# Performance work log

Measured on AMD Instinct MI355X. Metric: run time of the kernel, lower is better.

The kernel has to match this reference:

```python
import jax, jax.numpy as jnp
import numpy as np

N = 100000
E = 1600000
IN_DIM, HID_DIM, LAT_DIM = 256, 128, 64


def glorot(key, shape):
    lim = float(np.sqrt(6.0 / (shape[0] + shape[1])))
    return jax.random.uniform(key, shape, jnp.float32, -lim, lim)


def setup_inputs() -> dict:
    key = jax.random.key(0)
    ks = jax.random.split(key, 8)
    x = jax.random.normal(ks[0], (N, IN_DIM), jnp.float32)
    edge_index = jax.random.randint(ks[1], (2, E), 0, N, jnp.int64)
    return {
        "x": x,
        "edge_index": edge_index,
        "W1": glorot(ks[2], (IN_DIM, HID_DIM)),
        "b1": jnp.zeros((HID_DIM,), jnp.float32),
        "Wmu": glorot(ks[3], (HID_DIM, LAT_DIM)),
        "bmu": jnp.zeros((LAT_DIM,), jnp.float32),
        "Wls": glorot(ks[4], (HID_DIM, LAT_DIM)),
        "bls": jnp.zeros((LAT_DIM,), jnp.float32),
    }


def gcn_conv(x, src, dst, norm, W, b, n_nodes):
    # PyG GCNConv: linear transform, then symmetric-normalized scatter-add
    h = x @ W                                   # [N, out]
    msg = h[src] * norm[:, None]                # [E+N, out] gathered messages
    out = jax.ops.segment_sum(msg, dst, num_segments=n_nodes)
    return out + b


def reference(x, edge_index, W1, b1, Wmu, bmu, Wls, bls):
    # add self-loops (GCNConv default)
    loop = jnp.arange(N, dtype=edge_index.dtype)
    src = jnp.concatenate([edge_index[0], loop])
    dst = jnp.concatenate([edge_index[1], loop])
    # symmetric degree normalization: deg computed on target nodes
    deg = jax.ops.segment_sum(jnp.ones_like(dst, jnp.float32), dst, num_segments=N)
    dinv = jnp.where(deg > 0, jax.lax.rsqrt(jnp.maximum(deg, 1.0)), 0.0)
    norm = dinv[src] * dinv[dst]                # [E+N]

    h = jax.nn.relu(gcn_conv(x, src, dst, norm, W1, b1, N))
    mu = gcn_conv(h, src, dst, norm, Wmu, bmu, N)
    logstd = gcn_conv(h, src, dst, norm, Wls, bls, N)
    return (mu, logstd)
```

## Files before the change

### kernel.cpp

```cpp
#include <hip/hip_runtime.h>

#define IN_DIM 256
#define HID    128
#define LAT    64
#define SLOTS  64
#define RANGE  200
#define MAXBKT 512

typedef __attribute__((ext_vector_type(8))) short short8;
typedef __attribute__((ext_vector_type(4))) float floatx4;
typedef __attribute__((ext_vector_type(4))) int  intx4;
typedef __attribute__((ext_vector_type(2))) int  intx2;

static __device__ __forceinline__ ushort f2bf(float f) {
    union { float f; uint u; } v; v.f = f;
    uint u = v.u;
    uint r = (u + 0x7fffu + ((u >> 16) & 1u)) >> 16;
    return (ushort)r;
}
static __device__ __forceinline__ float bf_lo(uint v) { return __uint_as_float(v << 16); }
static __device__ __forceinline__ float bf_hi(uint v) { return __uint_as_float(v & 0xffff0000u); }

__global__ __launch_bounds__(256) void scatter_gemm1_kernel(
        const int* __restrict__ src, const int* __restrict__ dst,
        int* __restrict__ bkt, int* __restrict__ bkt_cnt,
        int cap, int nbkt, int E, int sblocks,
        const float* __restrict__ X, const ushort* __restrict__ W1T,
        ushort* __restrict__ O, int N) {
    __shared__ __align__(16) char smem[28 * 1024];

    if ((int)blockIdx.x < sblocks) {
        int* cntL  = (int*)smem;
        int* baseL = cntL + MAXBKT;
        int* posL  = baseL + MAXBKT;
        const int t = threadIdx.x;
        for (int b = t; b < nbkt; b += 256) { cntL[b] = 0; posL[b] = 0; }
        __syncthreads();
        const int e0 = blockIdx.x * 2048 + t * 8;
        int s[8], d[8];
        if (e0 + 7 < E) {
            *(int4*)(s)     = *(const int4*)(src + e0);
            *(int4*)(s + 4) = *(const int4*)(src + e0 + 4);
            *(int4*)(d)     = *(const int4*)(dst + e0);
            *(int4*)(d + 4) = *(const int4*)(dst + e0 + 4);
        } else {
            #pragma unroll
            for (int k = 0; k < 8; ++k) {
                int e = e0 + k;
                s[k] = (e < E) ? src[e] : 0;
                d[k] = (e < E) ? dst[e] : -1;
            }
        }
        int r[8];
        #pragma unroll
        for (int k = 0; k < 8; ++k) {
            r[k] = (d[k] >= 0) ? (d[k] / RANGE) : -1;
            if (r[k] >= 0) atomicAdd(&cntL[r[k]], 1);
        }
        __syncthreads();
        for (int b = t; b < nbkt; b += 256) {
            int c = cntL[b];
            baseL[b] = c ? atomicAdd(&bkt_cnt[b], c) : 0;
        }
        __syncthreads();
        #pragma unroll
        for (int k = 0; k < 8; ++k) {
            if (r[k] >= 0) {
                int off = atomicAdd(&posL[r[k]], 1);
                int p = baseL[r[k]] + off;
                if (p < cap) {
                    *(intx2*)(bkt + ((size_t)r[k] * cap + p) * 2) =
                        (intx2){s[k], d[k]};
                }
            }
        }
        return;
    }

    ushort* As = (ushort*)smem;
    ushort* Bs = As + 64 * 32;
    ushort* Cs = Bs + 128 * 32;
    const int bid  = blockIdx.x - sblocks;
    const int tid  = threadIdx.x;
    const int wave = tid >> 6, lane = tid & 63;
    const int q = lane >> 4, ln = lane & 15;
    const int row0 = bid * 64;
    floatx4 acc[8] = {};

    for (int k0 = 0; k0 < IN_DIM; k0 += 32) {
        #pragma unroll
        for (int t = 0; t < 2; ++t) {
            int j = t * 256 + tid;
            int r = j >> 3, kc = (j & 7) * 4;
            float4 v = make_float4(0.f, 0.f, 0.f, 0.f);
            if (row0 + r < N)
                v = *(const float4*)(X + (size_t)(row0 + r) * IN_DIM + k0 + kc);
            *(ushort4*)(As + r * 32 + kc) =
                make_ushort4(f2bf(v.x), f2bf(v.y), f2bf(v.z), f2bf(v.w));
        }
        #pragma unroll
        for (int t = 0; t < 2; ++t) {
            int c = t * 256 + tid;
            int n = c >> 2, kc = (c & 3) * 8;
            *(int4*)(Bs + n * 32 + kc) = *(const int4*)(W1T + (size_t)n * IN_DIM + k0 + kc);
        }
        __syncthreads();
        short8 a = *(const short8*)(As + (wave * 16 + ln) * 32 + q * 8);
        #pragma unroll
        for (int t = 0; t < 8; ++t) {
            short8 b = *(const short8*)(Bs + (t * 16 + ln) * 32 + q * 8);
            acc[t] = __builtin_amdgcn_mfma_f32_16x16x32_bf16(a, b, acc[t], 0, 0, 0);
        }
        __syncthreads();
    }
    #pragma unroll
    for (int t = 0; t < 8; ++t)
        #pragma unroll
        for (int r = 0; r < 4; ++r)
            Cs[(wave * 16 + q * 4 + r) * 128 + t * 16 + ln] = f2bf(acc[t][r]);
    __syncthreads();
    #pragma unroll
    for (int t = 0; t < 4; ++t) {
        int j = t * 256 + tid;
        int r = j >> 4, c8 = (j & 15) * 8;
        if (row0 + r < N)
            *(int4*)(O + (size_t)(row0 + r) * HID + c8) = *(const int4*)(Cs + r * 128 + c8);
    }
}

__global__ __launch_bounds__(256) void fill_bin_kernel(const int* __restrict__ bkt,
                                                       const int* __restrict__ bkt_cnt,
                                                       int* __restrict__ cur,
                                                       float* __restrict__ dinv,
                                                       int* __restrict__ csr,
                                                       int cap, int N) {
    __shared__ int lcnt[RANGE];
    __shared__ int lslots[RANGE * SLOTS];
    const int r  = blockIdx.x;
    const int lo = r * RANGE;
    const int R  = min(RANGE, N - lo);
    if (R <= 0) return;
    for (int j = threadIdx.x; j < R; j += 256) lcnt[j] = 0;
    __syncthreads();
    const int sz = min(bkt_cnt[r], cap);
    const int* b = bkt + (size_t)r * cap * 2;
    for (int i = threadIdx.x; i < sz; i += 256) {
        intx2 e = __builtin_nontemporal_load((const intx2*)(b + (size_t)i * 2));
        int ln = e.y - lo;
        int p = atomicAdd(&lcnt[ln], 1);
        if (p < SLOTS) lslots[(ln << 6) + p] = e.x;
    }
    __syncthreads();
    const int nInt4 = R << 4;
    int4* dstp = (int4*)(csr + ((size_t)lo << 6));
    const int4* srcp = (const int4*)lslots;
    for (int j = threadIdx.x; j < nInt4; j += 256)
        dstp[j] = srcp[j];
    for (int j = threadIdx.x; j < R; j += 256) {
        int c = lcnt[j];
        cur[lo + j]  = c;
        dinv[lo + j] = rsqrtf((float)(c + 1));
    }
}

__global__ void prep_weights(const float* __restrict__ W1, const float* __restrict__ Wmu,
                             const float* __restrict__ Wls,
                             ushort* __restrict__ W1T, ushort* __restrict__ W2T) {
    int idx = blockIdx.x * 256 + threadIdx.x;
    if (idx < IN_DIM * HID) {
        int n = idx & 127, k = idx >> 7;
        W1T[n * IN_DIM + k] = f2bf(W1[idx]);
    } else {
        int j = idx - IN_DIM * HID;
        if (j < HID * LAT) {
            int n = j & 63, k = j >> 6;
            W2T[n * HID + k] = f2bf(Wmu[j]);
        } else {
            int jj = j - HID * LAT;
            int n = jj & 63, k = jj >> 6;
            W2T[(64 + n) * HID + k] = f2bf(Wls[jj]);
        }
    }
}

__global__ __launch_bounds__(256) void agg_kernel(const ushort* __restrict__ in,
                                                  ushort* __restrict__ out,
                                                  const int* __restrict__ cnt,
                                                  const int* __restrict__ csr,
                                                  const float* __restrict__ dinv,
                                                  const float* __restrict__ bias,
                                                  int N, int mode) {
    int wid  = (blockIdx.x * 256 + threadIdx.x) >> 6;
    int lane = threadIdx.x & 63;
    if (wid >= N) return;
    const int cn   = min(cnt[wid], SLOTS);
    const float dd = dinv[wid];
    int e    = (cn > 0) ? csr[(wid << 6) + min(lane, cn - 1)] : wid;
    float nr = dinv[e] * dd;
    const int q    = lane >> 4;
    const int boff = (lane & 15) * 8;
    const ushort* inb = in + boff;
    float a0=0.f,a1=0.f,a2=0.f,a3=0.f,a4=0.f,a5=0.f,a6=0.f,a7=0.f;
    const int nfull = cn >> 2;
    int jj = 0;
    for (; jj + 2 <= nfull; jj += 2) {
        int j0 = (jj << 2) + q, j1 = j0 + 4;
        int   s0 = __shfl(e,  j0);
        int   s1 = __shfl(e,  j1);
        float n0 = __shfl(nr, j0);
        float n1 = __shfl(nr, j1);
        uint4 v0 = *(const uint4*)(inb + (size_t)s0 * HID);
        uint4 v1 = *(const uint4*)(inb + (size_t)s1 * HID);
        a0 += bf_lo(v0.x) * n0; a1 += bf_hi(v0.x) * n0;
        a2 += bf_lo(v0.y) * n0; a3 += bf_hi(v0.y) * n0;
        a4 += bf_lo(v0.z) * n0; a5 += bf_hi(v0.z) * n0;
        a6 += bf_lo(v0.w) * n0; a7 += bf_hi(v0.w) * n0;
        a0 += bf_lo(v1.x) * n1; a1 += bf_hi(v1.x) * n1;
        a2 += bf_lo(v1.y) * n1; a3 += bf_hi(v1.y) * n1;
        a4 += bf_lo(v1.z) * n1; a5 += bf_hi(v1.z) * n1;
        a6 += bf_lo(v1.w) * n1; a7 += bf_hi(v1.w) * n1;
    }
    if (jj < nfull) {
        int j0 = (jj << 2) + q;
        int   s0 = __shfl(e,  j0);
        float n0 = __shfl(nr, j0);
        uint4 v0 = *(const uint4*)(inb + (size_t)s0 * HID);
        a0 += bf_lo(v0.x) * n0; a1 += bf_hi(v0.x) * n0;
        a2 += bf_lo(v0.y) * n0; a3 += bf_hi(v0.y) * n0;
        a4 += bf_lo(v0.z) * n0; a5 += bf_hi(v0.z) * n0;
        a6 += bf_lo(v0.w) * n0; a7 += bf_hi(v0.w) * n0;
    }
    {
        int rem = cn - (nfull << 2);
        int jT  = max(min((nfull << 2) + q, cn - 1), 0);
        int   sT = __shfl(e,  jT);
        float nT = __shfl(nr, jT);
        if (q < rem) {
            uint4 v0 = *(const uint4*)(inb + (size_t)sT * HID);
            a0 += bf_lo(v0.x) * nT; a1 += bf_hi(v0.x) * nT;
            a2 += bf_lo(v0.y) * nT; a3 += bf_hi(v0.y) * nT;
            a4 += bf_lo(v0.z) * nT; a5 += bf_hi(v0.z) * nT;
            a6 += bf_lo(v0.w) * nT; a7 += bf_hi(v0.w) * nT;
        }
    }
    a0 += __shfl_xor(a0, 16); a1 += __shfl_xor(a1, 16);
    a2 += __shfl_xor(a2, 16); a3 += __shfl_xor(a3, 16);
    a4 += __shfl_xor(a4, 16); a5 += __shfl_xor(a5, 16);
    a6 += __shfl_xor(a6, 16); a7 += __shfl_xor(a7, 16);
    a0 += __shfl_xor(a0, 32); a1 += __shfl_xor(a1, 32);
    a2 += __shfl_xor(a2, 32); a3 += __shfl_xor(a3, 32);
    a4 += __shfl_xor(a4, 32); a5 += __shfl_xor(a5, 32);
    a6 += __shfl_xor(a6, 32); a7 += __shfl_xor(a7, 32);
    if (q == 0) {
        {
            uint4 sv = *(const uint4*)(in + (size_t)wid * HID + boff);
            float ss = dd * dd;
            a0 += bf_lo(sv.x) * ss; a1 += bf_hi(sv.x) * ss;
            a2 += bf_lo(sv.y) * ss; a3 += bf_hi(sv.y) * ss;
            a4 += bf_lo(sv.z) * ss; a5 += bf_hi(sv.z) * ss;
            a6 += bf_lo(sv.w) * ss; a7 += bf_hi(sv.w) * ss;
        }
        if (mode) {
            float4 b0 = *(const float4*)(bias + boff);
            float4 b1 = *(const float4*)(bias + boff + 4);
            a0 = fmaxf(a0 + b0.x, 0.f); a1 = fmaxf(a1 + b0.y, 0.f);
            a2 = fmaxf(a2 + b0.z, 0.f); a3 = fmaxf(a3 + b0.w, 0.f);
            a4 = fmaxf(a4 + b1.x, 0.f); a5 = fmaxf(a5 + b1.y, 0.f);
            a6 = fmaxf(a6 + b1.z, 0.f); a7 = fmaxf(a7 + b1.w, 0.f);
        }
        uint4 pk;
        pk.x = (uint)f2bf(a0) | ((uint)f2bf(a1) << 16);
        pk.y = (uint)f2bf(a2) | ((uint)f2bf(a3) << 16);
        pk.z = (uint)f2bf(a4) | ((uint)f2bf(a5) << 16);
        pk.w = (uint)f2bf(a6) | ((uint)f2bf(a7) << 16);
        *(uint4*)(out + (size_t)wid * HID + boff) = pk;
    }
}

__global__ __launch_bounds__(256) void gemm2_mfma(const ushort* __restrict__ G,
                                                  const ushort* __restrict__ W2T,
                                                  const float* __restrict__ bmu,
                                                  const float* __restrict__ bls,
                                                  float* __restrict__ mu,
                                                  float* __restrict__ ls, int N) {
    __shared__ ushort As[64 * 32];
    __shared__ ushort Bs[128 * 32];
    __shared__ float  Cs[64 * 128];
    const int tid  = threadIdx.x;
    const int wave = tid >> 6, lane = tid & 63;
    const int q = lane >> 4, ln = lane & 15;
    const int row0 = blockIdx.x * 64;
    floatx4 acc[8] = {};

    for (int k0 = 0; k0 < HID; k0 += 32) {
        {
            int r = tid >> 2, kc = (tid & 3) * 8;
            int4 v = make_int4(0, 0, 0, 0);
            if (row0 + r < N) v = *(const int4*)(G + (size_t)(row0 + r) * HID + k0 + kc);
            *(int4*)(As + r * 32 + kc) = v;
        }
        #pragma unroll
        for (int t = 0; t < 2; ++t) {
            int c = t * 256 + tid;
            int n = c >> 2, kc = (c & 3) * 8;
            *(int4*)(Bs + n * 32 + kc) = *(const int4*)(W2T + (size_t)n * HID + k0 + kc);
        }
        __syncthreads();
        short8 a = *(const short8*)(As + (wave * 16 + ln) * 32 + q * 8);
        #pragma unroll
        for (int t = 0; t < 8; ++t) {
            short8 b = *(const short8*)(Bs + (t * 16 + ln) * 32 + q * 8);
            acc[t] = __builtin_amdgcn_mfma_f32_16x16x32_bf16(a, b, acc[t], 0, 0, 0);
        }
        __syncthreads();
    }
    #pragma unroll
    for (int t = 0; t < 8; ++t)
        #pragma unroll
        for (int r = 0; r < 4; ++r)
            Cs[(wave * 16 + q * 4 + r) * 128 + t * 16 + ln] = acc[t][r];
    __syncthreads();
    #pragma unroll
    for (int t = 0; t < 8; ++t) {
        int j = t * 256 + tid;
        int r = j >> 5, c4 = (j & 31) * 4;
        if (row0 + r < N) {
            float4 v = *(const float4*)(Cs + r * 128 + c4);
            if (c4 < 64) {
                float4 b = *(const float4*)(bmu + c4);
                *(float4*)(mu + (size_t)(row0 + r) * LAT + c4) =
                    make_float4(v.x + b.x, v.y + b.y, v.z + b.z, v.w + b.w);
            } else {
                float4 b = *(const float4*)(bls + (c4 - 64));
                *(float4*)(ls + (size_t)(row0 + r) * LAT + (c4 - 64)) =
                    make_float4(v.x + b.x, v.y + b.y, v.z + b.z, v.w + b.w);
            }
        }
    }
}

extern "C" void kernel_launch(void* const* d_in, const int* in_sizes, int n_in,
                              void* d_out, int out_size, void* d_ws, size_t ws_size,
                              hipStream_t stream) {
    const float* x    = (const float*)d_in[0];
    const int*   edge = (const int*)d_in[1];
    const float* W1   = (const float*)d_in[2];
    const float* b1   = (const float*)d_in[3];
    const float* Wmu  = (const float*)d_in[4];
    const float* bmu  = (const float*)d_in[5];
    const float* Wls  = (const float*)d_in[6];
    const float* bls  = (const float*)d_in[7];

    const int N    = in_sizes[0] / IN_DIM;
    const int E    = in_sizes[1] / 2;
    const int nbkt = (N + RANGE - 1) / RANGE;
    const int cap  = 4096;

    const int* src = edge;
    const int* dst = edge + E;

    ushort* t1b  = (ushort*)d_ws;
    ushort* hb   = t1b + (size_t)N * HID;
    int*    csr  = (int*)(hb + (size_t)N * HID);
    int*    bkt  = (int*)(csr + (size_t)N * SLOTS);
    float*  dinv = (float*)(bkt + (size_t)MAXBKT * cap * 2);
    int*    cur  = (int*)(dinv + N);
    int* bkt_cnt = cur + N;
    ushort* W1T  = (ushort*)(bkt_cnt + MAXBKT);
    ushort* W2T  = W1T + IN_DIM * HID;
    ushort* gb   = t1b;

    float* mu = (float*)d_out;
    float* ls = mu + (size_t)N * LAT;

    (void)hipMemsetAsync(bkt_cnt, 0, (size_t)MAXBKT * sizeof(int), stream);

    prep_weights<<<(IN_DIM * HID + 2 * HID * LAT) / 256, 256, 0, stream>>>(W1, Wmu, Wls, W1T, W2T);

    {
        int sblocks  = (E + 2047) / 2048;
        int g1blocks = (N + 63) / 64;
        scatter_gemm1_kernel<<<sblocks + g1blocks, 256, 0, stream>>>(
            src, dst, bkt, bkt_cnt, cap, nbkt, E, sblocks, x, W1T, t1b, N);
    }

    fill_bin_kernel<<<nbkt, 256, 0, stream>>>(bkt, bkt_cnt, cur, dinv, csr, cap, N);

    {
        int blocks = (int)(((long long)N * 64 + 255) / 256);
        agg_kernel<<<blocks, 256, 0, stream>>>(t1b, hb, cur, csr, dinv, b1, N, 1);
    }
    {
        int blocks = (int)(((long long)N * 64 + 255) / 256);
        agg_kernel<<<blocks, 256, 0, stream>>>(hb, gb, cur, csr, dinv, nullptr, N, 0);
    }

    gemm2_mfma<<<(N + 63) / 64, 256, 0, stream>>>(gb, W2T, bmu, bls, mu, ls, N);
}
```

Baseline: 374.0 us.

## Fuse second aggregation into GEMM2 via swizzled LDS tile; reuse bucket atomics

```diff
diff --git a/kernel.cpp b/kernel.cpp
--- a/kernel.cpp
+++ b/kernel.cpp
@@ -32,9 +32,8 @@
     if ((int)blockIdx.x < sblocks) {
         int* cntL  = (int*)smem;
         int* baseL = cntL + MAXBKT;
-        int* posL  = baseL + MAXBKT;
         const int t = threadIdx.x;
-        for (int b = t; b < nbkt; b += 256) { cntL[b] = 0; posL[b] = 0; }
+        for (int b = t; b < nbkt; b += 256) cntL[b] = 0;
         __syncthreads();
         const int e0 = blockIdx.x * 2048 + t * 8;
         int s[8], d[8];
@@ -51,11 +50,11 @@
                 d[k] = (e < E) ? dst[e] : -1;
             }
         }
-        int r[8];
+        int r[8], off[8];
         #pragma unroll
         for (int k = 0; k < 8; ++k) {
             r[k] = (d[k] >= 0) ? (d[k] / RANGE) : -1;
-            if (r[k] >= 0) atomicAdd(&cntL[r[k]], 1);
+            if (r[k] >= 0) off[k] = atomicAdd(&cntL[r[k]], 1);
         }
         __syncthreads();
         for (int b = t; b < nbkt; b += 256) {
@@ -66,8 +65,7 @@
         #pragma unroll
         for (int k = 0; k < 8; ++k) {
             if (r[k] >= 0) {
-                int off = atomicAdd(&posL[r[k]], 1);
-                int p = baseL[r[k]] + off;
+                int p = baseL[r[k]] + off[k];
                 if (p < cap) {
                     *(intx2*)(bkt + ((size_t)r[k] * cap + p) * 2) =
                         (intx2){s[k], d[k]};
@@ -189,7 +187,7 @@
                                                   const int* __restrict__ csr,
                                                   const float* __restrict__ dinv,
                                                   const float* __restrict__ bias,
-                                                  int N, int mode) {
+                                                  int N) {
     int wid  = (blockIdx.x * 256 + threadIdx.x) >> 6;
     int lane = threadIdx.x & 63;
     if (wid >= N) return;
@@ -260,14 +258,12 @@
             a4 += bf_lo(sv.z) * ss; a5 += bf_hi(sv.z) * ss;
             a6 += bf_lo(sv.w) * ss; a7 += bf_hi(sv.w) * ss;
         }
-        if (mode) {
-            float4 b0 = *(const float4*)(bias + boff);
-            float4 b1 = *(const float4*)(bias + boff + 4);
-            a0 = fmaxf(a0 + b0.x, 0.f); a1 = fmaxf(a1 + b0.y, 0.f);
-            a2 = fmaxf(a2 + b0.z, 0.f); a3 = fmaxf(a3 + b0.w, 0.f);
-            a4 = fmaxf(a4 + b1.x, 0.f); a5 = fmaxf(a5 + b1.y, 0.f);
-            a6 = fmaxf(a6 + b1.z, 0.f); a7 = fmaxf(a7 + b1.w, 0.f);
-        }
+        float4 b0 = *(const float4*)(bias + boff);
+        float4 b1 = *(const float4*)(bias + boff + 4);
+        a0 = fmaxf(a0 + b0.x, 0.f); a1 = fmaxf(a1 + b0.y, 0.f);
+        a2 = fmaxf(a2 + b0.z, 0.f); a3 = fmaxf(a3 + b0.w, 0.f);
+        a4 = fmaxf(a4 + b1.x, 0.f); a5 = fmaxf(a5 + b1.y, 0.f);
+        a6 = fmaxf(a6 + b1.z, 0.f); a7 = fmaxf(a7 + b1.w, 0.f);
         uint4 pk;
         pk.x = (uint)f2bf(a0) | ((uint)f2bf(a1) << 16);
         pk.y = (uint)f2bf(a2) | ((uint)f2bf(a3) << 16);
@@ -277,63 +273,121 @@
     }
 }
 
-__global__ __launch_bounds__(256) void gemm2_mfma(const ushort* __restrict__ G,
-                                                  const ushort* __restrict__ W2T,
-                                                  const float* __restrict__ bmu,
-                                                  const float* __restrict__ bls,
-                                                  float* __restrict__ mu,
-                                                  float* __restrict__ ls, int N) {
-    __shared__ ushort As[64 * 32];
-    __shared__ ushort Bs[128 * 32];
-    __shared__ float  Cs[64 * 128];
+__global__ __launch_bounds__(256) void agg2_gemm2_kernel(
+        const ushort* __restrict__ in,
+        const int* __restrict__ cnt, const int* __restrict__ csr,
+        const float* __restrict__ dinv,
+        const ushort* __restrict__ W2T,
+        const float* __restrict__ bmu, const float* __restrict__ bls,
+        float* __restrict__ mu, float* __restrict__ ls, int N) {
+    __shared__ ushort Ag[64 * 128];
     const int tid  = threadIdx.x;
     const int wave = tid >> 6, lane = tid & 63;
     const int q = lane >> 4, ln = lane & 15;
     const int row0 = blockIdx.x * 64;
+    const int boff = ln * 8;
+
+    for (int i = 0; i < 16; ++i) {
+        const int lrow = wave * 16 + i;
+        const int wid  = row0 + lrow;
+        if (wid >= N) break;
+        const int cn   = min(cnt[wid], SLOTS);
+        const float dd = dinv[wid];
+        int e    = (cn > 0) ? csr[(wid << 6) + min(lane, cn - 1)] : wid;
+        float nr = dinv[e] * dd;
+        const ushort* inb = in + boff;
+        float a0=0.f,a1=0.f,a2=0.f,a3=0.f,a4=0.f,a5=0.f,a6=0.f,a7=0.f;
+        const int nfull = cn >> 2;
+        int jj = 0;
+        for (; jj + 2 <= nfull; jj += 2) {
+            int j0 = (jj << 2) + q, j1 = j0 + 4;
+            int   s0 = __shfl(e,  j0);
+            int   s1 = __shfl(e,  j1);
+            float n0 = __shfl(nr, j0);
+            float n1 = __shfl(nr, j1);
+            uint4 v0 = *(const uint4*)(inb + (size_t)s0 * HID);
+            uint4 v1 = *(const uint4*)(inb + (size_t)s1 * HID);
+            a0 += bf_lo(v0.x) * n0; a1 += bf_hi(v0.x) * n0;
+            a2 += bf_lo(v0.y) * n0; a3 += bf_hi(v0.y) * n0;
+            a4 += bf_lo(v0.z) * n0; a5 += bf_hi(v0.z) * n0;
+            a6 += bf_lo(v0.w) * n0; a7 += bf_hi(v0.w) * n0;
+            a0 += bf_lo(v1.x) * n1; a1 += bf_hi(v1.x) * n1;
+            a2 += bf_lo(v1.y) * n1; a3 += bf_hi(v1.y) * n1;
+            a4 += bf_lo(v1.z) * n1; a5 += bf_hi(v1.z) * n1;
+            a6 += bf_lo(v1.w) * n1; a7 += bf_hi(v1.w) * n1;
+        }
+        if (jj < nfull) {
+            int j0 = (jj << 2) + q;
+            int   s0 = __shfl(e,  j0);
+            float n0 = __shfl(nr, j0);
+            uint4 v0 = *(const uint4*)(inb + (size_t)s0 * HID);
+            a0 += bf_lo(v0.x) * n0; a1 += bf_hi(v0.x) * n0;
+            a2 += bf_lo(v0.y) * n0; a3 += bf_hi(v0.y) * n0;
+            a4 += bf_lo(v0.z) * n0; a5 += bf_hi(v0.z) * n0;
+            a6 += bf_lo(v0.w) * n0; a7 += bf_hi(v0.w) * n0;
+        }
+        {
+            int rem = cn - (nfull << 2);
+            int jT  = max(min((nfull << 2) + q, cn - 1), 0);
+            int   sT = __shfl(e,  jT);
+            float nT = __shfl(nr, jT);
+            if (q < rem) {
+                uint4 v0 = *(const uint4*)(inb + (size_t)sT * HID);
+                a0 += bf_lo(v0.x) * nT; a1 += bf_hi(v0.x) * nT;
+                a2 += bf_lo(v0.y) * nT; a3 += bf_hi(v0.y) * nT;
+                a4 += bf_lo(v0.z) * nT; a5 += bf_hi(v0.z) * nT;
+                a6 += bf_lo(v0.w) * nT; a7 += bf_hi(v0.w) * nT;
+            }
+        }
+        a0 += __shfl_xor(a0, 16); a1 += __shfl_xor(a1, 16);
+        a2 += __shfl_xor(a2, 16); a3 += __shfl_xor(a3, 16);
+        a4 += __shfl_xor(a4, 16); a5 += __shfl_xor(a5, 16);
+        a6 += __shfl_xor(a6, 16); a7 += __shfl_xor(a7, 16);
+        a0 += __shfl_xor(a0, 32); a1 += __shfl_xor(a1, 32);
+        a2 += __shfl_xor(a2, 32); a3 += __shfl_xor(a3, 32);
+        a4 += __shfl_xor(a4, 32); a5 += __shfl_xor(a5, 32);
+        a6 += __shfl_xor(a6, 32); a7 += __shfl_xor(a7, 32);
+        if (q == 0) {
+            uint4 sv = *(const uint4*)(in + (size_t)wid * HID + boff);
+            float ss = dd * dd;
+            a0 += bf_lo(sv.x) * ss; a1 += bf_hi(sv.x) * ss;
+            a2 += bf_lo(sv.y) * ss; a3 += bf_hi(sv.y) * ss;
+            a4 += bf_lo(sv.z) * ss; a5 += bf_hi(sv.z) * ss;
+            a6 += bf_lo(sv.w) * ss; a7 += bf_hi(sv.w) * ss;
+            uint4 pk;
+            pk.x = (uint)f2bf(a0) | ((uint)f2bf(a1) << 16);
+            pk.y = (uint)f2bf(a2) | ((uint)f2bf(a3) << 16);
+            pk.z = (uint)f2bf(a4) | ((uint)f2bf(a5) << 16);
+            pk.w = (uint)f2bf(a6) | ((uint)f2bf(a7) << 16);
+            int bc = (boff * 2) ^ ((lrow & 7) << 4);
+            *(uint4*)((char*)Ag + lrow * 256 + bc) = pk;
+        }
+    }
+    __syncthreads();
+
     floatx4 acc[8] = {};
-
-    for (int k0 = 0; k0 < HID; k0 += 32) {
-        {
-            int r = tid >> 2, kc = (tid & 3) * 8;
-            int4 v = make_int4(0, 0, 0, 0);
-            if (row0 + r < N) v = *(const int4*)(G + (size_t)(row0 + r) * HID + k0 + kc);
-            *(int4*)(As + r * 32 + kc) = v;
-        }
-        #pragma unroll
-        for (int t = 0; t < 2; ++t) {
-            int c = t * 256 + tid;
-            int n = c >> 2, kc = (c & 3) * 8;
-            *(int4*)(Bs + n * 32 + kc) = *(const int4*)(W2T + (size_t)n * HID + k0 + kc);
-        }
-        __syncthreads();
-        short8 a = *(const short8*)(As + (wave * 16 + ln) * 32 + q * 8);
+    const int ar = wave * 16 + ln;
+    #pragma unroll
+    for (int c = 0; c < 4; ++c) {
+        int bcA = ((c * 64) + q * 16) ^ ((ar & 7) << 4);
+        short8 a = *(const short8*)((const char*)Ag + ar * 256 + bcA);
         #pragma unroll
         for (int t = 0; t < 8; ++t) {
-            short8 b = *(const short8*)(Bs + (t * 16 + ln) * 32 + q * 8);
+            short8 b = *(const short8*)(W2T + (size_t)(t * 16 + ln) * HID + c * 32 + q * 8);
             acc[t] = __builtin_amdgcn_mfma_f32_16x16x32_bf16(a, b, acc[t], 0, 0, 0);
         }
-        __syncthreads();
-    }
-    #pragma unroll
-    for (int t = 0; t < 8; ++t)
-        #pragma unroll
-        for (int r = 0; r < 4; ++r)
-            Cs[(wave * 16 + q * 4 + r) * 128 + t * 16 + ln] = acc[t][r];
-    __syncthreads();
+    }
     #pragma unroll
     for (int t = 0; t < 8; ++t) {
-        int j = t * 256 + tid;
-        int r = j >> 5, c4 = (j & 31) * 4;
-        if (row0 + r < N) {
-            float4 v = *(const float4*)(Cs + r * 128 + c4);
-            if (c4 < 64) {
-                float4 b = *(const float4*)(bmu + c4);
-                *(float4*)(mu + (size_t)(row0 + r) * LAT + c4) =
-                    make_float4(v.x + b.x, v.y + b.y, v.z + b.z, v.w + b.w);
-            } else {
-                float4 b = *(const float4*)(bls + (c4 - 64));
-                *(float4*)(ls + (size_t)(row0 + r) * LAT + (c4 - 64)) =
-                    make_float4(v.x + b.x, v.y + b.y, v.z + b.z, v.w + b.w);
+        int col = t * 16 + ln;
+        float bv = (col < 64) ? bmu[col] : bls[col - 64];
+        #pragma unroll
+        for (int r = 0; r < 4; ++r) {
+            int row = row0 + wave * 16 + q * 4 + r;
+            if (row < N) {
+                float v = acc[t][r] + bv;
+                if (col < 64) mu[(size_t)row * LAT + col] = v;
+                else          ls[(size_t)row * LAT + (col - 64)] = v;
             }
         }
     }
@@ -368,7 +422,6 @@
     int* bkt_cnt = cur + N;
     ushort* W1T  = (ushort*)(bkt_cnt + MAXBKT);
     ushort* W2T  = W1T + IN_DIM * HID;
-    ushort* gb   = t1b;
 
     float* mu = (float*)d_out;
     float* ls = mu + (size_t)N * LAT;
@@ -388,12 +441,11 @@
 
     {
         int blocks = (int)(((long long)N * 64 + 255) / 256);
-        agg_kernel<<<blocks, 256, 0, stream>>>(t1b, hb, cur, csr, dinv, b1, N, 1);
-    }
+        agg_kernel<<<blocks, 256, 0, stream>>>(t1b, hb, cur, csr, dinv, b1, N);
+    }
+
     {
-        int blocks = (int)(((long long)N * 64 + 255) / 256);
-        agg_kernel<<<blocks, 256, 0, stream>>>(hb, gb, cur, csr, dinv, nullptr, N, 0);
-    }
-
-    gemm2_mfma<<<(N + 63) / 64, 256, 0, stream>>>(gb, W2T, bmu, bls, mu, ls, N);
-}
+        int blocks = (N + 63) / 64;
+        agg2_gemm2_kernel<<<blocks, 256, 0, stream>>>(hb, cur, csr, dinv, W2T, bmu, bls, mu, ls, N);
+    }
+}
```

After: 419.2 us. 12.1% more time.
